# Kernel tuning notes

Hardware: AMD Instinct MI355X
Metric: run time of the kernel (lower is better)

The kernel has to match this reference:

```python
import jax, jax.numpy as jnp
import numpy as np

DIM, HEADS, PAIR_DIM = 256, 8, 128
B, S, N = 1, 128, 256
DH = DIM // HEADS
SCALE = DH ** -0.5
EPS = 1e-5


def setup_inputs() -> dict:
    key = jax.random.key(0)
    ks = jax.random.split(key, 12)
    s = lambda fan_in: 1.0 / np.sqrt(fan_in)
    return {
        "msa": jax.random.normal(ks[0], (B, S, N, DIM), jnp.float32),
        "pair": jax.random.normal(ks[1], (B, N, N, PAIR_DIM), jnp.float32),
        "mask": jax.random.randint(ks[2], (B, N, N), 0, 2, jnp.int32),
        "Wqkv": jax.random.normal(ks[3], (3 * DIM, DIM), jnp.float32) * s(DIM),
        "bqkv": jnp.zeros((3 * DIM,), jnp.float32),
        "Wout": jax.random.normal(ks[4], (DIM, DIM), jnp.float32) * s(DIM),
        "bout": jnp.zeros((DIM,), jnp.float32),
        "Wpb": jax.random.normal(ks[5], (HEADS, PAIR_DIM), jnp.float32) * s(PAIR_DIM),
        "bpb": jnp.zeros((HEADS,), jnp.float32),
        "gamma": jnp.ones((DIM,), jnp.float32),
        "beta": jnp.zeros((DIM,), jnp.float32),
    }


def reference(msa, pair, mask, Wqkv, bqkv, Wout, bout, Wpb, bpb, gamma, beta):
    # qkv projection: [B,S,N,3*DIM] -> [B,S,N,3,H,DH]
    qkv = (msa @ Wqkv.T + bqkv).reshape(B, S, N, 3, HEADS, DH)
    q, k, v = qkv[..., 0, :, :], qkv[..., 1, :, :], qkv[..., 2, :, :]
    # scores [B,S,H,N,N]
    attn = jnp.einsum('bsnhc,bsmhc->bshnm', q, k) * SCALE
    attn = jnp.where(mask[:, None, None, :, :] == 0, -1e9, attn)
    # pair bias: [B,N,N,P] -> [B,1,H,N,N]
    pair_bias = (pair @ Wpb.T + bpb).transpose(0, 3, 1, 2)[:, None]
    attn = jax.nn.softmax(attn + pair_bias, axis=-1)
    out = jnp.einsum('bshnm,bsmhc->bsnhc', attn, v).reshape(B, S, N, DIM)
    out = out @ Wout.T + bout
    # residual + layernorm
    x = msa + out
    mu = jnp.mean(x, axis=-1, keepdims=True)
    var = jnp.var(x, axis=-1, keepdims=True)
    return (x - mu) * jax.lax.rsqrt(var + EPS) * gamma + beta
```

## Files before the change

### kernel.cpp

```cpp
#include <hip/hip_runtime.h>
#include <cstdint>
#include <cstddef>

typedef unsigned short u16;
typedef __bf16 bf16x8 __attribute__((ext_vector_type(8)));
typedef float f32x4 __attribute__((ext_vector_type(4)));
typedef unsigned int u32x4 __attribute__((ext_vector_type(4)));

#define SCALE_QK_LOG2 0.25509904f
#define INV_LN2 1.4426950408889634f

__device__ __forceinline__ u16 f2bf(float f){ return __builtin_bit_cast(u16, (__bf16)f); }
__device__ __forceinline__ float bf2f(u16 u){ unsigned v = ((unsigned)u)<<16; return __builtin_bit_cast(float, v); }
__device__ __forceinline__ bf16x8 ldfrag_g(const u16* p){
  return __builtin_bit_cast(bf16x8, *reinterpret_cast<const u32x4*>(p));
}
__device__ __forceinline__ void gload16(const u16* g, u16* lds){
  __builtin_amdgcn_global_load_lds((const __attribute__((address_space(1))) unsigned int*)g,
                                   (__attribute__((address_space(3))) unsigned int*)lds, 16, 0, 0);
}

__global__ __launch_bounds__(256) void k_cvt(const float* __restrict__ src,
                                             u16* __restrict__ dst, int n4){
  int stride = gridDim.x * blockDim.x;
  for (int idx = blockIdx.x*blockDim.x + threadIdx.x; idx < n4; idx += stride){
    float4 v = reinterpret_cast<const float4*>(src)[idx];
    ushort4 o;
    o.x = f2bf(v.x); o.y = f2bf(v.y); o.z = f2bf(v.z); o.w = f2bf(v.w);
    reinterpret_cast<ushort4*>(dst)[idx] = o;
  }
}

__global__ __launch_bounds__(256) void k_cvt2(const float* __restrict__ a, u16* __restrict__ da,
                                              const float* __restrict__ b, u16* __restrict__ db){
  int bid = blockIdx.x;
  if (bid < 192){
    int idx = bid*256 + threadIdx.x;
    float4 v = reinterpret_cast<const float4*>(a)[idx];
    ushort4 o; o.x=f2bf(v.x); o.y=f2bf(v.y); o.z=f2bf(v.z); o.w=f2bf(v.w);
    reinterpret_cast<ushort4*>(da)[idx] = o;
  } else {
    int idx = (bid-192)*256 + threadIdx.x;
    float4 v = reinterpret_cast<const float4*>(b)[idx];
    ushort4 o; o.x=f2bf(v.x); o.y=f2bf(v.y); o.z=f2bf(v.z); o.w=f2bf(v.w);
    reinterpret_cast<ushort4*>(db)[idx] = o;
  }
}

__global__ __launch_bounds__(256) void k_pair_bias(const float* __restrict__ pair,
        const int* __restrict__ mask, const float* __restrict__ Wpb,
        const float* __restrict__ bpb, u16* __restrict__ bT){
  __shared__ float wsm[8][128];
  __shared__ float bsm[8];
  int tid = threadIdx.x;
  for (int i = tid; i < 1024; i += 256) wsm[i>>7][i&127] = Wpb[i];
  if (tid < 8) bsm[tid] = bpb[tid];
  __syncthreads();
  int g = tid>>4, l = tid&15;
  int row = blockIdx.x*16 + g;
  const float4* p = reinterpret_cast<const float4*>(pair + (size_t)row*128);
  float4 a0 = p[l];
  float4 a1 = p[l+16];
  int c0 = 4*l, c1 = 64 + 4*l;
  float acc[8];
#pragma unroll
  for (int hh=0; hh<8; hh++){
    acc[hh] = a0.x*wsm[hh][c0] + a0.y*wsm[hh][c0+1] + a0.z*wsm[hh][c0+2] + a0.w*wsm[hh][c0+3]
            + a1.x*wsm[hh][c1] + a1.y*wsm[hh][c1+1] + a1.z*wsm[hh][c1+2] + a1.w*wsm[hh][c1+3];
  }
#pragma unroll
  for (int hh=0; hh<8; hh++){
    float v = acc[hh];
    v += __shfl_xor(v,1); v += __shfl_xor(v,2); v += __shfl_xor(v,4); v += __shfl_xor(v,8);
    acc[hh] = v;
  }
  if (l == 0){
    float mb = (mask[row] == 0) ? -1e9f : 0.0f;
    int n = row>>8, m = row&255;
#pragma unroll
    for (int hh=0; hh<8; hh++)
      bT[hh*65536 + m*256 + n] = f2bf((acc[hh] + bsm[hh] + mb) * INV_LN2);
  }
}

__global__ __launch_bounds__(256, 3) void k_qkv(const u16* __restrict__ A,
                                                const u16* __restrict__ B,
                                                const float* __restrict__ bq,
                                                u16* __restrict__ qkv){
  __shared__ __align__(16) u16 Al[128*64];
  __shared__ __align__(16) u16 Bl[128*64];
  const int tid = threadIdx.x;
  const int w = tid>>6, l = tid&63;
  const int wm = w>>1, wn = w&1;
  const int m0 = blockIdx.y*128, n0 = blockIdx.x*128;
  const int lr = l&15, lg = l>>4;
  f32x4 acc[4][4] = {};
  for (int kt=0; kt<4; ++kt){
    const int k0 = kt*64;
    __syncthreads();
#pragma unroll
    for (int j=0;j<4;j++){
      int ch = w*256 + j*64 + l;
      int r = ch>>3, sl = ch&7;
      gload16(A + (size_t)(m0+r)*256 + k0 + ((sl^(r&7))*8), Al + (size_t)(w*256 + j*64)*8);
      gload16(B + (size_t)(n0+r)*256 + k0 + ((sl^(r&7))*8), Bl + (size_t)(w*256 + j*64)*8);
    }
    __syncthreads();
#pragma unroll
    for (int ks=0; ks<2; ++ks){
      bf16x8 af[4], bfr[4];
#pragma unroll
      for (int t=0;t<4;t++){
        int ra = wm*64 + t*16 + lr;
        int sa = (ks*4 + lg) ^ (ra&7);
        af[t] = __builtin_bit_cast(bf16x8, *reinterpret_cast<const u32x4*>(&Al[ra*64 + sa*8]));
        int rb = wn*64 + t*16 + lr;
        int sb = (ks*4 + lg) ^ (rb&7);
        bfr[t] = __builtin_bit_cast(bf16x8, *reinterpret_cast<const u32x4*>(&Bl[rb*64 + sb*8]));
      }
#pragma unroll
      for (int tm=0;tm<4;tm++)
#pragma unroll
        for (int tn=0;tn<4;tn++)
          acc[tm][tn] = __builtin_amdgcn_mfma_f32_16x16x32_bf16(af[tm], bfr[tn], acc[tm][tn], 0,0,0);
    }
  }
#pragma unroll
  for (int tn=0;tn<4;tn++){
    int c = n0 + wn*64 + tn*16 + lr;
    int t3 = c>>8, hh = (c>>5)&7, dh = c&31;
    float bb = bq[c];
    u16* obase = qkv + (size_t)(t3*8+hh)*32768*32 + dh;
#pragma unroll
    for (int tm=0;tm<4;tm++){
#pragma unroll
      for (int rr=0;rr<4;rr++){
        int m = m0 + wm*64 + tm*16 + lg*4 + rr;
        obase[(size_t)m*32] = f2bf(acc[tm][tn][rr] + bb);
      }
    }
  }
}

__global__ __launch_bounds__(256, 2) void k_attn(const u16* __restrict__ qkv,
                                                 const u16* __restrict__ bT,
                                                 u16* __restrict__ O){
  __shared__ __align__(16) u16 vT[32*256];
  __shared__ __align__(16) u16 P[4][32*64];
  const int h = blockIdx.x, s = blockIdx.y, z = blockIdx.z;
  const int tid = threadIdx.x;
  const int w = tid>>6, l = tid&63;
  const int lr = l&15, lg = l>>4;
  const int n0 = z*128 + 32*w;
  const u16* qb = qkv + ((size_t)h*32768 + s*256)*32;
  const u16* kb = qkv + ((size_t)(8+h)*32768 + s*256)*32;
  const u16* vb = qkv + ((size_t)(16+h)*32768 + s*256)*32;
  const u16* bb = bT + h*65536;

#pragma unroll
  for (int i=0;i<4;i++){
    int flat4 = tid + 256*i;
    int m = flat4>>2, d0 = (flat4&3)*8;
    u32x4 d = *reinterpret_cast<const u32x4*>(vb + (size_t)m*32 + d0);
    u16 tmp[8];
    *reinterpret_cast<u32x4*>(tmp) = d;
#pragma unroll
    for (int j=0;j<8;j++){
      int dh = d0 + j;
      vT[dh*256 + (((m>>3)^(dh&7))*8) + (m&7)] = tmp[j];
    }
  }
  __syncthreads();

  bf16x8 qf[2];
#pragma unroll
  for (int t=0;t<2;t++)
    qf[t] = ldfrag_g(qb + (size_t)(n0 + t*16 + lr)*32 + lg*8);

  f32x4 sacc[2][16] = {};
#pragma unroll
  for (int kt=0; kt<4; ++kt){
    bf16x8 kf[4];
#pragma unroll
    for (int tn=0;tn<4;tn++)
      kf[tn] = ldfrag_g(kb + (size_t)(kt*64 + tn*16 + lr)*32 + lg*8);
#pragma unroll
    for (int t=0;t<2;t++)
#pragma unroll
      for (int tn=0;tn<4;tn++)
        sacc[t][kt*4+tn] = __builtin_amdgcn_mfma_f32_16x16x32_bf16(qf[t], kf[tn], sacc[t][kt*4+tn], 0,0,0);
  }

#pragma unroll
  for (int kt=0;kt<4;kt++){
#pragma unroll
    for (int t=0;t<2;t++)
#pragma unroll
      for (int tn=0;tn<4;tn++){
        ushort4 b4 = *reinterpret_cast<const ushort4*>(
            bb + (size_t)(kt*64 + tn*16 + lr)*256 + n0 + t*16 + lg*4);
        float bc[4] = { bf2f(b4.x), bf2f(b4.y), bf2f(b4.z), bf2f(b4.w) };
#pragma unroll
        for (int rr=0;rr<4;rr++)
          sacc[t][kt*4+tn][rr] = sacc[t][kt*4+tn][rr]*SCALE_QK_LOG2 + bc[rr];
      }
  }

  float inv_l[2][4];
#pragma unroll
  for (int t=0;t<2;t++){
#pragma unroll
    for (int rr=0;rr<4;rr++){
      float mx = sacc[t][0][rr];
#pragma unroll
      for (int j=1;j<16;j++) mx = fmaxf(mx, sacc[t][j][rr]);
      mx = fmaxf(mx, __shfl_xor(mx,1));
      mx = fmaxf(mx, __shfl_xor(mx,2));
      mx = fmaxf(mx, __shfl_xor(mx,4));
      mx = fmaxf(mx, __shfl_xor(mx,8));
      float ps = 0.f;
#pragma unroll
      for (int j=0;j<16;j++){
        float p = __builtin_amdgcn_exp2f(sacc[t][j][rr] - mx);
        sacc[t][j][rr] = p;
        ps += p;
      }
      ps += __shfl_xor(ps,1);
      ps += __shfl_xor(ps,2);
      ps += __shfl_xor(ps,4);
      ps += __shfl_xor(ps,8);
      inv_l[t][rr] = 1.0f / ps;
    }
  }

  f32x4 oacc[2][2] = {};
#pragma unroll
  for (int mt=0; mt<4; ++mt){
#pragma unroll
    for (int t=0;t<2;t++){
#pragma unroll
      for (int rr=0;rr<4;rr++){
        int row = t*16 + lg*4 + rr;
        int rb = row*64;
        int sx = row&7;
#pragma unroll
        for (int tn=0;tn<4;tn++){
          int col = tn*16 + lr;
          P[w][rb + (((col>>3)^sx)*8) + (col&7)] = f2bf(sacc[t][mt*4+tn][rr]);
        }
      }
    }
#pragma unroll
    for (int kk=0;kk<2;kk++){
      bf16x8 vf[2];
#pragma unroll
      for (int dt=0;dt<2;dt++){
        int c = dt*16 + lr;
        int slot = (mt*8 + kk*4 + lg) ^ (c&7);
        vf[dt] = __builtin_bit_cast(bf16x8, *reinterpret_cast<const u32x4*>(&vT[c*256 + slot*8]));
      }
#pragma unroll
      for (int t=0;t<2;t++){
        int ra = t*16 + lr;
        int sa = (kk*4 + lg) ^ (ra&7);
        bf16x8 pf = __builtin_bit_cast(bf16x8, *reinterpret_cast<const u32x4*>(&P[w][ra*64 + sa*8]));
        oacc[t][0] = __builtin_amdgcn_mfma_f32_16x16x32_bf16(pf, vf[0], oacc[t][0], 0,0,0);
        oacc[t][1] = __builtin_amdgcn_mfma_f32_16x16x32_bf16(pf, vf[1], oacc[t][1], 0,0,0);
      }
    }
  }
#pragma unroll
  for (int t=0;t<2;t++){
#pragma unroll
    for (int rr=0;rr<4;rr++){
      int n = n0 + t*16 + lg*4 + rr;
      float inv = inv_l[t][rr];
      size_t rowb = (size_t)(s*256 + n)*256 + h*32;
#pragma unroll
      for (int dt=0;dt<2;dt++)
        O[rowb + dt*16 + lr] = f2bf(oacc[t][dt][rr]*inv);
    }
  }
}

__global__ __launch_bounds__(256, 3) void k_out_ln(const u16* __restrict__ A,
        const u16* __restrict__ Wo, const float* __restrict__ bo,
        const float* __restrict__ msa, const float* __restrict__ gamma,
        const float* __restrict__ beta, float* __restrict__ out){
  __shared__ __align__(16) u16 Al[64*64];
  __shared__ __align__(16) u16 Wl[256*64];
  __shared__ float redS[64][4];
  __shared__ float redQ[64][4];
  const int tid = threadIdx.x;
  const int w = tid>>6, l = tid&63;
  const int lr = l&15, lg = l>>4;
  const int m0 = blockIdx.x*64;
  f32x4 acc[4][4] = {};
  for (int kt=0;kt<4;kt++){
    const int k0 = kt*64;
    __syncthreads();
#pragma unroll
    for (int j=0;j<2;j++){
      int ch = w*128 + j*64 + l;
      int r = ch>>3, sl = ch&7;
      gload16(A + (size_t)(m0+r)*256 + k0 + ((sl^(r&7))*8), Al + (size_t)(w*128 + j*64)*8);
    }
#pragma unroll
    for (int j=0;j<8;j++){
      int ch = w*512 + j*64 + l;
      int r = ch>>3, sl = ch&7;
      gload16(Wo + (size_t)r*256 + k0 + ((sl^(r&7))*8), Wl + (size_t)(w*512 + j*64)*8);
    }
    __syncthreads();
#pragma unroll
    for (int ks=0;ks<2;ks++){
      bf16x8 af[4], bfr[4];
#pragma unroll
      for (int t=0;t<4;t++){
        int ra = t*16 + lr;
        int sa = (ks*4+lg) ^ (ra&7);
        af[t] = __builtin_bit_cast(bf16x8, *reinterpret_cast<const u32x4*>(&Al[ra*64 + sa*8]));
        int rb = w*64 + t*16 + lr;
        int sb = (ks*4+lg) ^ (rb&7);
        bfr[t] = __builtin_bit_cast(bf16x8, *reinterpret_cast<const u32x4*>(&Wl[rb*64 + sb*8]));
      }
#pragma unroll
      for (int tm=0;tm<4;tm++)
#pragma unroll
        for (int tn=0;tn<4;tn++)
          acc[tm][tn] = __builtin_amdgcn_mfma_f32_16x16x32_bf16(af[tm], bfr[tn], acc[tm][tn], 0,0,0);
    }
  }
#pragma unroll
  for (int tn=0;tn<4;tn++){
    int c = w*64 + tn*16 + lr;
    float bc = bo[c];
#pragma unroll
    for (int tm=0;tm<4;tm++)
#pragma unroll
      for (int rr=0;rr<4;rr++){
        int m = m0 + tm*16 + lg*4 + rr;
        acc[tm][tn][rr] += bc + msa[(size_t)m*256 + c];
      }
  }
#pragma unroll
  for (int tm=0;tm<4;tm++){
#pragma unroll
    for (int rr=0;rr<4;rr++){
      float sS = 0.f, sQ = 0.f;
#pragma unroll
      for (int tn=0;tn<4;tn++){
        float v = acc[tm][tn][rr];
        sS += v; sQ += v*v;
      }
      sS += __shfl_xor(sS,1); sS += __shfl_xor(sS,2); sS += __shfl_xor(sS,4); sS += __shfl_xor(sS,8);
      sQ += __shfl_xor(sQ,1); sQ += __shfl_xor(sQ,2); sQ += __shfl_xor(sQ,4); sQ += __shfl_xor(sQ,8);
      if (lr == 0){
        int row = tm*16 + lg*4 + rr;
        redS[row][w] = sS;
        redQ[row][w] = sQ;
      }
    }
  }
  __syncthreads();
#pragma unroll
  for (int tm=0;tm<4;tm++){
#pragma unroll
    for (int rr=0;rr<4;rr++){
      int row = tm*16 + lg*4 + rr;
      float S = redS[row][0]+redS[row][1]+redS[row][2]+redS[row][3];
      float Q = redQ[row][0]+redQ[row][1]+redQ[row][2]+redQ[row][3];
      float mu = S * (1.0f/256.0f);
      float var = Q * (1.0f/256.0f) - mu*mu;
      float inv = rsqrtf(var + 1e-5f);
      int m = m0 + row;
#pragma unroll
      for (int tn=0;tn<4;tn++){
        int c = w*64 + tn*16 + lr;
        out[(size_t)m*256 + c] = (acc[tm][tn][rr]-mu)*inv*gamma[c] + beta[c];
      }
    }
  }
}

extern "C" void kernel_launch(void* const* d_in, const int* in_sizes, int n_in,
                              void* d_out, int out_size, void* d_ws, size_t ws_size,
                              hipStream_t stream) {
  const float* msa  = (const float*)d_in[0];
  const float* pair = (const float*)d_in[1];
  const int*   mask = (const int*)d_in[2];
  const float* Wqkv = (const float*)d_in[3];
  const float* bqkv = (const float*)d_in[4];
  const float* Wout = (const float*)d_in[5];
  const float* bout = (const float*)d_in[6];
  const float* Wpb  = (const float*)d_in[7];
  const float* bpb  = (const float*)d_in[8];
  const float* gamma= (const float*)d_in[9];
  const float* beta = (const float*)d_in[10];
  float* out = (float*)d_out;

  char* ws = (char*)d_ws;
  u16*   msa_bf  = (u16*)(ws);
  u16*   wqkv_bf = (u16*)(ws + 16777216);
  u16*   wout_bf = (u16*)(ws + 17170432);
  u16*   biasT   = (u16*)(ws + 17301504);
  u16*   qkvb    = (u16*)(ws + 18350080);
  u16*   Ob      = (u16*)(ws + 68681728);

  k_cvt<<<4096, 256, 0, stream>>>(msa, msa_bf, 8388608/4);
  k_cvt2<<<256, 256, 0, stream>>>(Wqkv, wqkv_bf, Wout, wout_bf);
  k_pair_bias<<<4096, 256, 0, stream>>>(pair, mask, Wpb, bpb, biasT);
  k_qkv<<<dim3(6,256), 256, 0, stream>>>(msa_bf, wqkv_bf, bqkv, qkvb);
  k_attn<<<dim3(8,128,2), 256, 0, stream>>>(qkvb, biasT, Ob);
  k_out_ln<<<512, 256, 0, stream>>>(Ob, wout_bf, bout, msa, gamma, beta, out);
}
```

Measured before the change: 233.4 us.

## Fuse msa bf16 conversion into QKV GEMM, merge prep kernels, widen attention blocks

The standalone msa fp32→bf16 conversion kernel is removed. The QKV GEMM now reads fp32 msa directly and converts it while staging the tile into LDS. The weight conversions and pair-bias kernels are merged into one launch. The attention kernel uses 512-thread blocks that cover all 256 query rows per (head, sequence), so the V transpose is loaded once per block instead of twice. This saves a full 16 MB write and reread plus launch overhead, but the GEMM A-tile load now goes through registers instead of direct global-to-LDS copies and moves twice the bytes, and the larger attention blocks may lower occupancy.

```diff
diff --git a/kernel.cpp b/kernel.cpp
--- a/kernel.cpp
+++ b/kernel.cpp
@@ -20,44 +20,35 @@
                                    (__attribute__((address_space(3))) unsigned int*)lds, 16, 0, 0);
 }
 
-__global__ __launch_bounds__(256) void k_cvt(const float* __restrict__ src,
-                                             u16* __restrict__ dst, int n4){
-  int stride = gridDim.x * blockDim.x;
-  for (int idx = blockIdx.x*blockDim.x + threadIdx.x; idx < n4; idx += stride){
-    float4 v = reinterpret_cast<const float4*>(src)[idx];
-    ushort4 o;
-    o.x = f2bf(v.x); o.y = f2bf(v.y); o.z = f2bf(v.z); o.w = f2bf(v.w);
-    reinterpret_cast<ushort4*>(dst)[idx] = o;
-  }
-}
-
-__global__ __launch_bounds__(256) void k_cvt2(const float* __restrict__ a, u16* __restrict__ da,
-                                              const float* __restrict__ b, u16* __restrict__ db){
+__global__ __launch_bounds__(256) void k_pre(const float* __restrict__ pair,
+        const int* __restrict__ mask, const float* __restrict__ Wpb,
+        const float* __restrict__ bpb, u16* __restrict__ bT,
+        const float* __restrict__ Wqkv, u16* __restrict__ wqkv_bf,
+        const float* __restrict__ Wout, u16* __restrict__ wout_bf){
   int bid = blockIdx.x;
-  if (bid < 192){
-    int idx = bid*256 + threadIdx.x;
-    float4 v = reinterpret_cast<const float4*>(a)[idx];
-    ushort4 o; o.x=f2bf(v.x); o.y=f2bf(v.y); o.z=f2bf(v.z); o.w=f2bf(v.w);
-    reinterpret_cast<ushort4*>(da)[idx] = o;
-  } else {
-    int idx = (bid-192)*256 + threadIdx.x;
-    float4 v = reinterpret_cast<const float4*>(b)[idx];
-    ushort4 o; o.x=f2bf(v.x); o.y=f2bf(v.y); o.z=f2bf(v.z); o.w=f2bf(v.w);
-    reinterpret_cast<ushort4*>(db)[idx] = o;
-  }
-}
-
-__global__ __launch_bounds__(256) void k_pair_bias(const float* __restrict__ pair,
-        const int* __restrict__ mask, const float* __restrict__ Wpb,
-        const float* __restrict__ bpb, u16* __restrict__ bT){
+  int tid = threadIdx.x;
+  if (bid >= 4096){
+    int cb = bid - 4096;
+    if (cb < 192){
+      int idx = cb*256 + tid;
+      float4 v = reinterpret_cast<const float4*>(Wqkv)[idx];
+      ushort4 o; o.x=f2bf(v.x); o.y=f2bf(v.y); o.z=f2bf(v.z); o.w=f2bf(v.w);
+      reinterpret_cast<ushort4*>(wqkv_bf)[idx] = o;
+    } else {
+      int idx = (cb-192)*256 + tid;
+      float4 v = reinterpret_cast<const float4*>(Wout)[idx];
+      ushort4 o; o.x=f2bf(v.x); o.y=f2bf(v.y); o.z=f2bf(v.z); o.w=f2bf(v.w);
+      reinterpret_cast<ushort4*>(wout_bf)[idx] = o;
+    }
+    return;
+  }
   __shared__ float wsm[8][128];
   __shared__ float bsm[8];
-  int tid = threadIdx.x;
   for (int i = tid; i < 1024; i += 256) wsm[i>>7][i&127] = Wpb[i];
   if (tid < 8) bsm[tid] = bpb[tid];
   __syncthreads();
   int g = tid>>4, l = tid&15;
-  int row = blockIdx.x*16 + g;
+  int row = bid*16 + g;
   const float4* p = reinterpret_cast<const float4*>(pair + (size_t)row*128);
   float4 a0 = p[l];
   float4 a1 = p[l+16];
@@ -83,7 +74,7 @@
   }
 }
 
-__global__ __launch_bounds__(256, 3) void k_qkv(const u16* __restrict__ A,
+__global__ __launch_bounds__(256, 3) void k_qkv(const float* __restrict__ Amsa,
                                                 const u16* __restrict__ B,
                                                 const float* __restrict__ bq,
                                                 u16* __restrict__ qkv){
@@ -100,10 +91,18 @@
     __syncthreads();
 #pragma unroll
     for (int j=0;j<4;j++){
-      int ch = w*256 + j*64 + l;
+      int ch = tid + 256*j;
       int r = ch>>3, sl = ch&7;
-      gload16(A + (size_t)(m0+r)*256 + k0 + ((sl^(r&7))*8), Al + (size_t)(w*256 + j*64)*8);
-      gload16(B + (size_t)(n0+r)*256 + k0 + ((sl^(r&7))*8), Bl + (size_t)(w*256 + j*64)*8);
+      const float* src = Amsa + (size_t)(m0+r)*256 + k0 + sl*8;
+      float4 x0 = reinterpret_cast<const float4*>(src)[0];
+      float4 x1 = reinterpret_cast<const float4*>(src)[1];
+      ushort4 lo, hi;
+      lo.x=f2bf(x0.x); lo.y=f2bf(x0.y); lo.z=f2bf(x0.z); lo.w=f2bf(x0.w);
+      hi.x=f2bf(x1.x); hi.y=f2bf(x1.y); hi.z=f2bf(x1.z); hi.w=f2bf(x1.w);
+      u16* dst = &Al[r*64 + ((sl^(r&7))*8)];
+      reinterpret_cast<ushort4*>(dst)[0] = lo;
+      reinterpret_cast<ushort4*>(dst)[1] = hi;
+      gload16(B + (size_t)(n0+r)*256 + k0 + ((sl^(r&7))*8), Bl + (size_t)(w*64 + 256*j)*8);
     }
     __syncthreads();
 #pragma unroll
@@ -142,24 +141,24 @@
   }
 }
 
-__global__ __launch_bounds__(256, 2) void k_attn(const u16* __restrict__ qkv,
+__global__ __launch_bounds__(512, 2) void k_attn(const u16* __restrict__ qkv,
                                                  const u16* __restrict__ bT,
                                                  u16* __restrict__ O){
   __shared__ __align__(16) u16 vT[32*256];
-  __shared__ __align__(16) u16 P[4][32*64];
-  const int h = blockIdx.x, s = blockIdx.y, z = blockIdx.z;
+  __shared__ __align__(16) u16 P[8][32*64];
+  const int h = blockIdx.x, s = blockIdx.y;
   const int tid = threadIdx.x;
   const int w = tid>>6, l = tid&63;
   const int lr = l&15, lg = l>>4;
-  const int n0 = z*128 + 32*w;
+  const int n0 = 32*w;
   const u16* qb = qkv + ((size_t)h*32768 + s*256)*32;
   const u16* kb = qkv + ((size_t)(8+h)*32768 + s*256)*32;
   const u16* vb = qkv + ((size_t)(16+h)*32768 + s*256)*32;
   const u16* bb = bT + h*65536;
 
 #pragma unroll
-  for (int i=0;i<4;i++){
-    int flat4 = tid + 256*i;
+  for (int i=0;i<2;i++){
+    int flat4 = tid + 512*i;
     int m = flat4>>2, d0 = (flat4&3)*8;
     u32x4 d = *reinterpret_cast<const u32x4*>(vb + (size_t)m*32 + d0);
     u16 tmp[8];
@@ -400,17 +399,14 @@
   float* out = (float*)d_out;
 
   char* ws = (char*)d_ws;
-  u16*   msa_bf  = (u16*)(ws);
-  u16*   wqkv_bf = (u16*)(ws + 16777216);
-  u16*   wout_bf = (u16*)(ws + 17170432);
-  u16*   biasT   = (u16*)(ws + 17301504);
-  u16*   qkvb    = (u16*)(ws + 18350080);
-  u16*   Ob      = (u16*)(ws + 68681728);
-
-  k_cvt<<<4096, 256, 0, stream>>>(msa, msa_bf, 8388608/4);
-  k_cvt2<<<256, 256, 0, stream>>>(Wqkv, wqkv_bf, Wout, wout_bf);
-  k_pair_bias<<<4096, 256, 0, stream>>>(pair, mask, Wpb, bpb, biasT);
-  k_qkv<<<dim3(6,256), 256, 0, stream>>>(msa_bf, wqkv_bf, bqkv, qkvb);
-  k_attn<<<dim3(8,128,2), 256, 0, stream>>>(qkvb, biasT, Ob);
+  u16*   wqkv_bf = (u16*)(ws);
+  u16*   wout_bf = (u16*)(ws + 393216);
+  u16*   biasT   = (u16*)(ws + 524288);
+  u16*   qkvb    = (u16*)(ws + 1572864);
+  u16*   Ob      = (u16*)(ws + 51904512);
+
+  k_pre<<<4352, 256, 0, stream>>>(pair, mask, Wpb, bpb, biasT, Wqkv, wqkv_bf, Wout, wout_bf);
+  k_qkv<<<dim3(6,256), 256, 0, stream>>>(msa, wqkv_bf, bqkv, qkvb);
+  k_attn<<<dim3(8,128), 512, 0, stream>>>(qkvb, biasT, Ob);
   k_out_ln<<<512, 256, 0, stream>>>(Ob, wout_bf, bout, msa, gamma, beta, out);
 }
```

Result: slower. 249.9 us (+7.1%).
